# Optimization experiments

Measured on AMD Instinct MI355X. Metric: run time of the kernel, lower is better.

The kernel has to match this reference:

```python
import jax, jax.numpy as jnp
import numpy as np

WINDOW_SIZE = 11
SIGMA = 1.5

def _gaussian_window():
    x = np.arange(WINDOW_SIZE, dtype=np.float64) - WINDOW_SIZE // 2
    g = np.exp(-(x ** 2) / (2.0 * SIGMA ** 2))
    g = (g / g.sum()).astype(np.float32)
    w2 = np.outer(g, g)  # [11, 11]
    return jnp.asarray(w2)


def setup_inputs() -> dict:
    key = jax.random.key(0)
    k1, k2 = jax.random.split(key)
    B, C, H, W = 32, 3, 512, 512
    img1 = jax.random.uniform(k1, (B, C, H, W), dtype=jnp.float32)
    img2 = jax.random.uniform(k2, (B, C, H, W), dtype=jnp.float32)
    return {"img1": img1, "img2": img2}


def reference(img1, img2):
    # peak = 1.0, size_average = True
    c1 = jnp.float32(0.01 ** 2)
    c2 = jnp.float32(0.03 ** 2)
    C = img1.shape[1]
    w2 = _gaussian_window()

    # One fused depthwise conv over the 5 statistic planes (same math as 5
    # separate grouped convs in the original).
    stacked = jnp.concatenate(
        [img1, img2, img1 * img1, img2 * img2, img1 * img2], axis=1
    )  # [B, 5C, H, W]
    kernel = jnp.tile(w2[None, None], (5 * C, 1, 1, 1))  # [5C, 1, 11, 11]
    out = jax.lax.conv_general_dilated(
        stacked, kernel,
        window_strides=(1, 1), padding='VALID',
        feature_group_count=5 * C,
        dimension_numbers=('NCHW', 'OIHW', 'NCHW'),
    )  # [B, 5C, H-10, W-10]

    mu1 = out[:, 0 * C:1 * C]
    mu2 = out[:, 1 * C:2 * C]
    mu1_sq = mu1 * mu1
    mu2_sq = mu2 * mu2
    mu1_mu2 = mu1 * mu2
    sigma1_sq = out[:, 2 * C:3 * C] - mu1_sq
    sigma2_sq = out[:, 3 * C:4 * C] - mu2_sq
    sigma12 = out[:, 4 * C:5 * C] - mu1_mu2

    ssim_map = ((2 * mu1_mu2 + c1) * (2 * sigma12 + c2)) / (
        (mu1_sq + mu2_sq + c1) * (sigma1_sq + sigma2_sq + c2)
    )
    return jnp.mean(ssim_map)
```

## Files before the change

### kernel.cpp

```cpp
#include <hip/hip_runtime.h>


namespace {
constexpr int IMG_H = 512, IMG_W = 512;
constexpr int OUT_H = 502, OUT_W = 502;
constexpr int NIMG  = 96;
constexpr int RPB   = 32;
constexpr int NBAND = 16;
constexpr int QR    = 3;
constexpr int BUFW  = 528;
constexpr int NTASK = NBAND * NIMG;
constexpr double TOTAL = 24192384.0;

constexpr double U0 = 0.0038659201;
constexpr double U1 = 0.0285655007;
constexpr double U2 = 0.1353352832366127;
constexpr double U3 = 0.4111122898;
constexpr double U4 = 0.8007374026;
constexpr double SS = 1.0 + 2.0 * (U0 + U1 + U2 + U3 + U4);
}

__device__ __forceinline__ int sw(int c4) { return c4 ^ ((c4 >> 3) & 1); }

__device__ __forceinline__ float2 f2fma(float w, float2 a, float2 c) {
    return make_float2(fmaf(w, a.x, c.x), fmaf(w, a.y, c.y));
}

__global__ __launch_bounds__(256, 4) void ssim_main(const float* __restrict__ img1,
                                                    const float* __restrict__ img2,
                                                    float* __restrict__ partial)
{
    __shared__ __align__(16) float vrow[QR][5][BUFW];
    __shared__ float red[4];

    const float g[11] = {
        (float)(U0/SS), (float)(U1/SS), (float)(U2/SS), (float)(U3/SS), (float)(U4/SS),
        (float)(1.0/SS),
        (float)(U4/SS), (float)(U3/SS), (float)(U2/SS), (float)(U1/SS), (float)(U0/SS)
    };
    constexpr float C1 = 1e-4f, C2 = 9e-4f;

    const int t   = threadIdx.x;
    const int z   = blockIdx.y;
    const int oy0 = blockIdx.x * RPB;
    const int row_end = min(oy0 + RPB, OUT_H);

    const float* p1 = img1 + (size_t)z * (IMG_H * IMG_W);
    const float* p2 = img2 + (size_t)z * (IMG_H * IMG_W);

    const int woff = (sw(t >> 1) << 2) + ((t & 1) << 1);

    const int hq = t >> 6;
    const int hl = t & 63;
    const int cb = hl << 3;
    int roff[5];
    #pragma unroll
    for (int k = 0; k < 5; ++k) roff[k] = sw((cb >> 2) + k) << 2;

    float local = 0.f;

    for (int r0 = oy0; r0 < row_end; r0 += QR) {
        float2 xr[QR + 10], yr[QR + 10];
        #pragma unroll
        for (int j = 0; j < QR + 10; ++j) {
            int row = r0 + j;
            row = row < IMG_H ? row : IMG_H - 1;
            xr[j] = *(const float2*)(p1 + (size_t)row * IMG_W + 2 * t);
            yr[j] = *(const float2*)(p2 + (size_t)row * IMG_W + 2 * t);
        }
        float2 vm1[QR], vm2[QR], v11[QR], v22[QR], v12[QR];
        #pragma unroll
        for (int q = 0; q < QR; ++q) {
            vm1[q] = make_float2(0.f, 0.f); vm2[q] = make_float2(0.f, 0.f);
            v11[q] = make_float2(0.f, 0.f); v22[q] = make_float2(0.f, 0.f);
            v12[q] = make_float2(0.f, 0.f);
        }
        #pragma unroll
        for (int j = 0; j < QR + 10; ++j) {
            float2 x = xr[j], y = yr[j];
            float2 xx = make_float2(x.x * x.x, x.y * x.y);
            float2 yy = make_float2(y.x * y.x, y.y * y.y);
            float2 xy = make_float2(x.x * y.x, x.y * y.y);
            #pragma unroll
            for (int q = 0; q < QR; ++q) {
                int k = j - q;
                if (k >= 0 && k < 11) {
                    float w = g[k];
                    vm1[q] = f2fma(w, x,  vm1[q]);
                    vm2[q] = f2fma(w, y,  vm2[q]);
                    v11[q] = f2fma(w, xx, v11[q]);
                    v22[q] = f2fma(w, yy, v22[q]);
                    v12[q] = f2fma(w, xy, v12[q]);
                }
            }
        }
        __syncthreads();
        #pragma unroll
        for (int q = 0; q < QR; ++q) {
            *(float2*)&vrow[q][0][woff] = vm1[q];
            *(float2*)&vrow[q][1][woff] = vm2[q];
            *(float2*)&vrow[q][2][woff] = v11[q];
            *(float2*)&vrow[q][3][woff] = v22[q];
            *(float2*)&vrow[q][4][woff] = v12[q];
        }
        __syncthreads();

        const int rr = r0 + hq;
        if (hq < QR && rr < row_end && cb < OUT_W) {
            float aa[5][8];
            #pragma unroll
            for (int ch = 0; ch < 5; ++ch) {
                const float* bc = &vrow[hq][ch][0];
                float f[20];
                #pragma unroll
                for (int k = 0; k < 5; ++k) {
                    float4 v = *(const float4*)(bc + roff[k]);
                    f[4*k+0] = v.x; f[4*k+1] = v.y; f[4*k+2] = v.z; f[4*k+3] = v.w;
                }
                #pragma unroll
                for (int j = 0; j < 8; ++j) {
                    float s = 0.f;
                    #pragma unroll
                    for (int k = 0; k < 11; ++k) s = fmaf(g[k], f[j + k], s);
                    aa[ch][j] = s;
                }
            }
            #pragma unroll
            for (int j = 0; j < 8; ++j) {
                if (cb + j < OUT_W) {
                    float mu1 = aa[0][j], mu2 = aa[1][j];
                    float mu11 = mu1 * mu1, mu22 = mu2 * mu2, mu12 = mu1 * mu2;
                    float s1  = aa[2][j] - mu11;
                    float s2  = aa[3][j] - mu22;
                    float s12 = aa[4][j] - mu12;
                    float num = fmaf(2.f, mu12, C1) * fmaf(2.f, s12, C2);
                    float den = (mu11 + mu22 + C1) * (s1 + s2 + C2);
                    float rc  = __builtin_amdgcn_rcpf(den);
                    rc = rc * fmaf(-den, rc, 2.f);
                    local += num * rc;
                }
            }
        }
    }

    #pragma unroll
    for (int off = 32; off > 0; off >>= 1) local += __shfl_down(local, off, 64);
    if ((t & 63) == 0) red[t >> 6] = local;
    __syncthreads();
    if (t == 0)
        partial[blockIdx.y * NBAND + blockIdx.x] = red[0] + red[1] + red[2] + red[3];
}

__global__ void ssim_fin(const float* __restrict__ partial, float* __restrict__ out)
{
    __shared__ double sd[256];
    double sum = 0.0;
    for (int i = threadIdx.x; i < NTASK; i += 256) sum += (double)partial[i];
    sd[threadIdx.x] = sum;
    __syncthreads();
    for (int w = 128; w > 0; w >>= 1) {
        if (threadIdx.x < w) sd[threadIdx.x] += sd[threadIdx.x + w];
        __syncthreads();
    }
    if (threadIdx.x == 0) out[0] = (float)(sd[0] / TOTAL);
}

extern "C" void kernel_launch(void* const* d_in, const int* in_sizes, int n_in,
                              void* d_out, int out_size, void* d_ws, size_t ws_size,
                              hipStream_t stream)
{
    (void)in_sizes; (void)n_in; (void)out_size; (void)ws_size;
    const float* img1 = (const float*)d_in[0];
    const float* img2 = (const float*)d_in[1];
    float* partial = (float*)d_ws;

    hipLaunchKernelGGL(ssim_main, dim3(NBAND, NIMG), dim3(256), 0, stream,
                       img1, img2, partial);
    hipLaunchKernelGGL(ssim_fin, dim3(1), dim3(256), 0, stream,
                       partial, (float*)d_out);
}
```

Before: 275.2 us.

## Process two rows per pass and spread horizontal pass over all threads

```diff
diff --git a/kernel.cpp b/kernel.cpp
--- a/kernel.cpp
+++ b/kernel.cpp
@@ -7,7 +7,7 @@
 constexpr int NIMG  = 96;
 constexpr int RPB   = 32;
 constexpr int NBAND = 16;
-constexpr int QR    = 3;
+constexpr int QR    = 2;
 constexpr int BUFW  = 528;
 constexpr int NTASK = NBAND * NIMG;
 constexpr double TOTAL = 24192384.0;
@@ -19,8 +19,6 @@
 constexpr double U4 = 0.8007374026;
 constexpr double SS = 1.0 + 2.0 * (U0 + U1 + U2 + U3 + U4);
 }
-
-__device__ __forceinline__ int sw(int c4) { return c4 ^ ((c4 >> 3) & 1); }
 
 __device__ __forceinline__ float2 f2fma(float w, float2 a, float2 c) {
     return make_float2(fmaf(w, a.x, c.x), fmaf(w, a.y, c.y));
@@ -48,55 +46,54 @@
     const float* p1 = img1 + (size_t)z * (IMG_H * IMG_W);
     const float* p2 = img2 + (size_t)z * (IMG_H * IMG_W);
 
-    const int woff = (sw(t >> 1) << 2) + ((t & 1) << 1);
+    const int woff = 2 * t;
 
-    const int hq = t >> 6;
-    const int hl = t & 63;
-    const int cb = hl << 3;
-    int roff[5];
-    #pragma unroll
-    for (int k = 0; k < 5; ++k) roff[k] = sw((cb >> 2) + k) << 2;
+    const int hq = t >> 7;
+    const int u  = t & 127;
+    const int cb = u << 2;
 
     float local = 0.f;
 
     for (int r0 = oy0; r0 < row_end; r0 += QR) {
-        float2 xr[QR + 10], yr[QR + 10];
+        float2 xr[12], yr[12];
         #pragma unroll
-        for (int j = 0; j < QR + 10; ++j) {
-            int row = r0 + j;
-            row = row < IMG_H ? row : IMG_H - 1;
-            xr[j] = *(const float2*)(p1 + (size_t)row * IMG_W + 2 * t);
-            yr[j] = *(const float2*)(p2 + (size_t)row * IMG_W + 2 * t);
+        for (int j = 0; j < 12; ++j) {
+            xr[j] = *(const float2*)(p1 + (size_t)(r0 + j) * IMG_W + 2 * t);
+            yr[j] = *(const float2*)(p2 + (size_t)(r0 + j) * IMG_W + 2 * t);
         }
-        float2 vm1[QR], vm2[QR], v11[QR], v22[QR], v12[QR];
+        float2 vm1[2], vm2[2], v11[2], v22[2], v12[2];
         #pragma unroll
-        for (int q = 0; q < QR; ++q) {
+        for (int q = 0; q < 2; ++q) {
             vm1[q] = make_float2(0.f, 0.f); vm2[q] = make_float2(0.f, 0.f);
             v11[q] = make_float2(0.f, 0.f); v22[q] = make_float2(0.f, 0.f);
             v12[q] = make_float2(0.f, 0.f);
         }
         #pragma unroll
-        for (int j = 0; j < QR + 10; ++j) {
+        for (int j = 0; j < 12; ++j) {
             float2 x = xr[j], y = yr[j];
             float2 xx = make_float2(x.x * x.x, x.y * x.y);
             float2 yy = make_float2(y.x * y.x, y.y * y.y);
             float2 xy = make_float2(x.x * y.x, x.y * y.y);
-            #pragma unroll
-            for (int q = 0; q < QR; ++q) {
-                int k = j - q;
-                if (k >= 0 && k < 11) {
-                    float w = g[k];
-                    vm1[q] = f2fma(w, x,  vm1[q]);
-                    vm2[q] = f2fma(w, y,  vm2[q]);
-                    v11[q] = f2fma(w, xx, v11[q]);
-                    v22[q] = f2fma(w, yy, v22[q]);
-                    v12[q] = f2fma(w, xy, v12[q]);
-                }
+            if (j < 11) {
+                float w = g[j];
+                vm1[0] = f2fma(w, x,  vm1[0]);
+                vm2[0] = f2fma(w, y,  vm2[0]);
+                v11[0] = f2fma(w, xx, v11[0]);
+                v22[0] = f2fma(w, yy, v22[0]);
+                v12[0] = f2fma(w, xy, v12[0]);
+            }
+            if (j >= 1) {
+                float w = g[j - 1];
+                vm1[1] = f2fma(w, x,  vm1[1]);
+                vm2[1] = f2fma(w, y,  vm2[1]);
+                v11[1] = f2fma(w, xx, v11[1]);
+                v22[1] = f2fma(w, yy, v22[1]);
+                v12[1] = f2fma(w, xy, v12[1]);
             }
         }
         __syncthreads();
         #pragma unroll
-        for (int q = 0; q < QR; ++q) {
+        for (int q = 0; q < 2; ++q) {
             *(float2*)&vrow[q][0][woff] = vm1[q];
             *(float2*)&vrow[q][1][woff] = vm2[q];
             *(float2*)&vrow[q][2][woff] = v11[q];
@@ -106,19 +103,19 @@
         __syncthreads();
 
         const int rr = r0 + hq;
-        if (hq < QR && rr < row_end && cb < OUT_W) {
-            float aa[5][8];
+        if (rr < row_end) {
+            float aa[5][4];
             #pragma unroll
             for (int ch = 0; ch < 5; ++ch) {
                 const float* bc = &vrow[hq][ch][0];
-                float f[20];
+                float f[16];
                 #pragma unroll
-                for (int k = 0; k < 5; ++k) {
-                    float4 v = *(const float4*)(bc + roff[k]);
+                for (int k = 0; k < 4; ++k) {
+                    float4 v = *(const float4*)(bc + ((u + k) << 2));
                     f[4*k+0] = v.x; f[4*k+1] = v.y; f[4*k+2] = v.z; f[4*k+3] = v.w;
                 }
                 #pragma unroll
-                for (int j = 0; j < 8; ++j) {
+                for (int j = 0; j < 4; ++j) {
                     float s = 0.f;
                     #pragma unroll
                     for (int k = 0; k < 11; ++k) s = fmaf(g[k], f[j + k], s);
@@ -126,7 +123,7 @@
                 }
             }
             #pragma unroll
-            for (int j = 0; j < 8; ++j) {
+            for (int j = 0; j < 4; ++j) {
                 if (cb + j < OUT_W) {
                     float mu1 = aa[0][j], mu2 = aa[1][j];
                     float mu11 = mu1 * mu1, mu22 = mu2 * mu2, mu12 = mu1 * mu2;
```

Result: slower. 312.8 us (+13.7%).
